# Kernel tuning notes

Hardware: AMD Instinct MI355X
Metric: run time of the kernel (lower is better)

Reference implementation:

```python
import jax, jax.numpy as jnp
import numpy as np

N, E = 20000, 320000
IN_DIM, EDGE_DIM, HID = 64, 16, 64
# (in_c, heads, channels, out_c) per layer; last layer heads=1, concat=False
DIMS = [(64, 4, 64, 256), (256, 4, 64, 256), (256, 1, 64, 64)]


def _ln(x, g, b):
    m = x.mean(-1, keepdims=True)
    v = x.var(-1, keepdims=True)
    return (x - m) / jnp.sqrt(v + 1e-5) * g + b


def _gatv2(x, ei, ea, Wl, bl, Wr, br, We, att, bc, concat):
    # PyG GATv2Conv, eval mode (no dropout), add_self_loops=True, fill_value='mean'
    n = x.shape[0]
    H, C = att.shape
    ar = jnp.arange(n, dtype=ei.dtype)
    src = jnp.concatenate([ei[0], ar])
    dst = jnp.concatenate([ei[1], ar])
    ea_f = jnp.concatenate([ea, jnp.broadcast_to(ea.mean(0), (n, ea.shape[1]))], 0)
    xl = (x @ Wl + bl).reshape(n, H, C)   # source transform
    xr = (x @ Wr + br).reshape(n, H, C)   # target transform
    ee = (ea_f @ We).reshape(-1, H, C)    # edge transform (no bias in PyG)
    e = jax.nn.leaky_relu(xl[src] + xr[dst] + ee, 0.2)       # [E+N, H, C]
    score = jnp.einsum('ehc,hc->eh', e, att)                 # [E+N, H]
    mx = jax.ops.segment_max(score, dst, num_segments=n)
    a = jnp.exp(score - mx[dst])
    a = a / (jax.ops.segment_sum(a, dst, num_segments=n)[dst] + 1e-16)
    out = jax.ops.segment_sum(a[:, :, None] * xl[src], dst, num_segments=n)  # [N,H,C]
    out = out.reshape(n, H * C) if concat else out.mean(1)
    return out + bc


def _forward(x, eis, eas, Wp, bp, gp, bep, layers):
    h = jax.nn.gelu(_ln(x @ Wp + bp, gp, bep), approximate=False)
    for i in range(3):
        Wl, bl, Wr, br, We, att, bc, g, be, Wsk, bsk = layers[i]
        res = h @ Wsk + bsk
        h = _gatv2(h, eis[i], eas[i], Wl, bl, Wr, br, We, att, bc, i < 2)
        h = jax.nn.gelu(_ln(h, g, be), approximate=False) + res
    return h


def setup_inputs() -> dict:
    key = jax.random.key(0)
    ks = iter(jax.random.split(key, 64))
    rn = lambda shape, s=0.05: jax.random.normal(next(ks), shape, jnp.float32) * s
    d = {'x': jax.random.normal(next(ks), (N, IN_DIM), jnp.float32)}
    for i in range(3):
        d['ei%d' % i] = jax.random.randint(next(ks), (2, E), 0, N, jnp.int32)
        d['ea%d' % i] = jax.random.normal(next(ks), (E, EDGE_DIM), jnp.float32)
    d['Wp'] = rn((IN_DIM, HID)); d['bp'] = jnp.zeros(HID)
    d['gp'] = jnp.ones(HID); d['bep'] = jnp.zeros(HID)
    for i, (ic, H, C, oc) in enumerate(DIMS):
        hc = H * C
        d['Wl%d' % i] = rn((ic, hc)); d['bl%d' % i] = jnp.zeros(hc)
        d['Wr%d' % i] = rn((ic, hc)); d['br%d' % i] = jnp.zeros(hc)
        d['We%d' % i] = rn((EDGE_DIM, hc))
        d['att%d' % i] = rn((H, C), 0.1)
        d['bc%d' % i] = jnp.zeros(hc if i < 2 else C)
        d['g%d' % i] = jnp.ones(oc); d['be%d' % i] = jnp.zeros(oc)
        d['Wsk%d' % i] = rn((ic, oc)); d['bsk%d' % i] = jnp.zeros(oc)
    return d


def reference(x, ei0, ea0, ei1, ea1, ei2, ea2, Wp, bp, gp, bep,
              Wl0, bl0, Wr0, br0, We0, att0, bc0, g0, be0, Wsk0, bsk0,
              Wl1, bl1, Wr1, br1, We1, att1, bc1, g1, be1, Wsk1, bsk1,
              Wl2, bl2, Wr2, br2, We2, att2, bc2, g2, be2, Wsk2, bsk2):
    layers = [
        (Wl0, bl0, Wr0, br0, We0, att0, bc0, g0, be0, Wsk0, bsk0),
        (Wl1, bl1, Wr1, br1, We1, att1, bc1, g1, be1, Wsk1, bsk1),
        (Wl2, bl2, Wr2, br2, We2, att2, bc2, g2, be2, Wsk2, bsk2),
    ]
    return _forward(x, (ei0, ei1, ei2), (ea0, ea1, ea2), Wp, bp, gp, bep, layers)
```

## Files before the change

kernel.cpp:

```cpp
#include <hip/hip_runtime.h>
#include <hip/hip_bf16.h>
#include <math.h>

#define NV 20000
#define NE 320000
#define CSR_PAD 16

typedef __attribute__((ext_vector_type(8))) short bf16x8;
typedef __attribute__((ext_vector_type(4))) float f32x4;
typedef __attribute__((ext_vector_type(2))) _Float16 h2;

static __device__ __forceinline__ ushort f2b(float f) {
  __hip_bfloat16 h = __float2bfloat16(f);
  return *reinterpret_cast<ushort*>(&h);
}
static __device__ __forceinline__ float b2f(ushort u) {
  union { ushort s[2]; float f; } c;
  c.s[0] = 0; c.s[1] = u;
  return c.f;
}
static __device__ __forceinline__ ushort f2h(float f) {
  _Float16 h = (_Float16)f;
  return *reinterpret_cast<ushort*>(&h);
}
static __device__ __forceinline__ float blo(unsigned u) { return __uint_as_float(u << 16); }
static __device__ __forceinline__ float bhi(unsigned u) { return __uint_as_float(u & 0xffff0000u); }
static __device__ __forceinline__ h2 u2h2(unsigned u) {
  union { unsigned v; h2 h; } c; c.v = u; return c.h;
}

static __device__ __forceinline__ float wave_sum64(float x) {
  x += __int_as_float(__builtin_amdgcn_update_dpp(0, __float_as_int(x), 0x111, 0xF, 0xF, true));
  x += __int_as_float(__builtin_amdgcn_update_dpp(0, __float_as_int(x), 0x112, 0xF, 0xF, true));
  x += __int_as_float(__builtin_amdgcn_update_dpp(0, __float_as_int(x), 0x114, 0xF, 0xF, true));
  x += __int_as_float(__builtin_amdgcn_update_dpp(0, __float_as_int(x), 0x118, 0xF, 0xF, true));
  x += __int_as_float(__builtin_amdgcn_update_dpp(0, __float_as_int(x), 0x142, 0xA, 0xF, true));
  x += __int_as_float(__builtin_amdgcn_update_dpp(0, __float_as_int(x), 0x143, 0xC, 0xF, true));
  return __int_as_float(__builtin_amdgcn_readlane(__float_as_int(x), 63));
}

static __device__ __forceinline__ float sum16(float x) {
  x += __int_as_float(__builtin_amdgcn_update_dpp(0, __float_as_int(x), 0x121, 0xF, 0xF, true));
  x += __int_as_float(__builtin_amdgcn_update_dpp(0, __float_as_int(x), 0x122, 0xF, 0xF, true));
  x += __int_as_float(__builtin_amdgcn_update_dpp(0, __float_as_int(x), 0x124, 0xF, 0xF, true));
  x += __int_as_float(__builtin_amdgcn_update_dpp(0, __float_as_int(x), 0x128, 0xF, 0xF, true));
  return x;
}

static __device__ __forceinline__ float dot16h_i(const uint4* __restrict__ E,
                                                 const h2* __restrict__ Wch,
                                                 float s) {
#if __has_builtin(__builtin_amdgcn_fdot2)
  const h2* e = (const h2*)E;
#pragma unroll
  for (int j = 0; j < 8; ++j) s = __builtin_amdgcn_fdot2(e[j], Wch[j], s, false);
  return s;
#else
  const unsigned* u = (const unsigned*)E;
#pragma unroll
  for (int j = 0; j < 8; ++j) {
    union { unsigned v; h2 h; } cv; cv.v = u[j];
    s = fmaf((float)cv.h[0], (float)Wch[j][0], s);
    s = fmaf((float)cv.h[1], (float)Wch[j][1], s);
  }
  return s;
#endif
}

struct HArgs {
  const int* ei[3]; int* counts;
  const float* ea[3]; float* easum[3];
};

__global__ __launch_bounds__(256) void hist_kernel(HArgs a) {
  const int t = threadIdx.x, b = (int)blockIdx.x;
  if (b < 3750) {
    int gi = b * 256 + t;
    int l = gi / NE, i = gi - l * NE;
    atomicAdd(&a.counts[(size_t)l * (NV + 1) + a.ei[l][NE + i]], 1);
  } else {
    const int cb = b - 3750;
    const int l = cb >> 8, blk = cb & 255;
    const float4* ea4 = (const float4*)a.ea[l];
    const int cg = t & 3;
    int r = blk * 64 + (t >> 2);
    const int rstride = 256 * 64;
    float4 s = make_float4(0.f, 0.f, 0.f, 0.f);
    for (; r < NE; r += rstride) {
      float4 v = ea4[(size_t)r * 4 + cg];
      s.x += v.x; s.y += v.y; s.z += v.z; s.w += v.w;
    }
    __shared__ float4 red4[256];
    red4[t] = s;
    __syncthreads();
    if (t < 4) {
      float4 tot = make_float4(0.f, 0.f, 0.f, 0.f);
      for (int j = t; j < 256; j += 4) {
        float4 v = red4[j];
        tot.x += v.x; tot.y += v.y; tot.z += v.z; tot.w += v.w;
      }
      atomicAdd(&a.easum[l][t * 4 + 0], tot.x);
      atomicAdd(&a.easum[l][t * 4 + 1], tot.y);
      atomicAdd(&a.easum[l][t * 4 + 2], tot.z);
      atomicAdd(&a.easum[l][t * 4 + 3], tot.w);
    }
  }
}

struct CJob { const float* src; ushort* dst; int K, M; };
struct K2Args {
  const int* counts; int* offs; int* cursor;
  CJob jobs[9];
  unsigned* csr[3]; ushort* eab[3];
  const float *x, *Wp, *bp, *gp, *bep;
  ushort* h0;
  const float* easum;
  const float* We[3];
  unsigned* wchx[3];
  float* esfO[3];
};

__global__ __launch_bounds__(1024) void scan_proj_kernel(K2Args a) {
  const int b = blockIdx.x, t = threadIdx.x;
  if (b < 3) {
    const int* counts = a.counts + b * (NV + 1);
    int* offs = a.offs + b * (NV + 1);
    int* cursor = a.cursor + b * NV;
    __shared__ int ws[16];
    __shared__ int wexcl[17];
    const int lane = t & 63, wid = t >> 6;
    const int base = t * 20;
    int v[20];
    int tot = 0;
#pragma unroll
    for (int j = 0; j < 20; ++j) {
      int i = base + j;
      v[j] = (i < NV) ? counts[i] : 0;
      tot += v[j];
    }
    int x = tot;
#pragma unroll
    for (int o = 1; o < 64; o <<= 1) {
      int yy = __shfl_up(x, o, 64);
      if (lane >= o) x += yy;
    }
    if (lane == 63) ws[wid] = x;
    __syncthreads();
    if (t == 0) {
      int r = 0;
#pragma unroll
      for (int j = 0; j < 16; ++j) { wexcl[j] = r; r += ws[j]; }
      wexcl[16] = r;
    }
    __syncthreads();
    int run = wexcl[wid] + (x - tot);
#pragma unroll
    for (int j = 0; j < 20; ++j) {
      int i = base + j;
      if (i < NV) { offs[i] = run; cursor[i] = run; }
      run += v[j];
    }
    if (t == 0) offs[NV] = wexcl[16];
  } else if (b < 19) {
    if (b == 3 && t < 3 * CSR_PAD) {
      int l = t >> 4, p = t & 15;
      a.csr[l][NE + p] = 0u;
      uint4 z = make_uint4(0, 0, 0, 0);
      *(uint4*)(a.eab[l] + (size_t)(NE + p) * 16) = z;
      *(uint4*)(a.eab[l] + (size_t)(NE + p) * 16 + 8) = z;
    }
#pragma unroll
    for (int j = 0; j < 9; ++j) {
      CJob jb = a.jobs[j];
      const int total = jb.M * jb.K;
      for (int i = (b - 3) * 1024 + t; i < total; i += 16 * 1024) {
        int m = i / jb.K, k = i - m * jb.K;
        jb.dst[i] = f2b(jb.src[(size_t)k * jb.M + m]);
      }
    }
  } else if (b < 19 + NV / 16) {
    const int wid = t >> 6, lane = t & 63;
    const int row = (b - 19) * 16 + wid;
    float xv = a.x[(size_t)row * 64 + lane];
    float acc = a.bp[lane];
#pragma unroll
    for (int k = 0; k < 64; ++k) {
      float v = __shfl(xv, k, 64);
      acc = fmaf(v, a.Wp[k * 64 + lane], acc);
    }
    float s1 = wave_sum64(acc), s2 = wave_sum64(acc * acc);
    float mean = s1 * (1.0f / 64.0f);
    float var  = s2 * (1.0f / 64.0f) - mean * mean;
    float yv = (acc - mean) * rsqrtf(var + 1e-5f) * a.gp[lane] + a.bep[lane];
    float gel = 0.5f * yv * (1.0f + erff(yv * 0.70710678118654752f));
    a.h0[(size_t)row * 64 + lane] = f2b(gel);
  } else {
    for (int i = t; i < 4608; i += 1024) {
      int l, e;
      if (i < 2048)      { l = 0; e = i; }
      else if (i < 4096) { l = 1; e = i - 2048; }
      else               { l = 2; e = i - 4096; }
      const int hcl = (l == 2) ? 64 : 256;
      int k8 = e / hcl, c = e - k8 * hcl;
      const float* We = a.We[l];
      a.wchx[l][e] = (unsigned)f2h(We[(2 * k8) * hcl + c]) |
                     ((unsigned)f2h(We[(2 * k8 + 1) * hcl + c]) << 16);
    }
    for (int i = t; i < 576; i += 1024) {
      int l, c;
      if (i < 256)      { l = 0; c = i; }
      else if (i < 512) { l = 1; c = i - 256; }
      else              { l = 2; c = i - 512; }
      const int hcl = (l == 2) ? 64 : 256;
      const float* We = a.We[l];
      const float* es = a.easum + l * 16;
      float s = 0.f;
#pragma unroll
      for (int k8 = 0; k8 < 8; ++k8) {
        s = fmaf(es[2 * k8], We[(2 * k8) * hcl + c], s);
        s = fmaf(es[2 * k8 + 1], We[(2 * k8 + 1) * hcl + c], s);
      }
      a.esfO[l][c] = s * (1.0f / (float)NE);
    }
  }
}

struct K3Args {
  const ushort *A, *WT;
  const float *b0, *b1, *b2;
  ushort *O0, *O1; float* O2;
  int K, M1, M2, Mtot, NT;
  const int* ei[3]; const float* ea[3];
  int* cursor;
  unsigned* csr[3]; ushort* eab[3]; int HC[3];
};

__global__ __launch_bounds__(256) void mega_kernel(K3Args a) {
  __shared__ ushort As[128][40];
  __shared__ ushort Bs[64][40];
  const int t = threadIdx.x;
  const int b = (int)blockIdx.x;
  if (b < a.NT) {
    const int wave = t >> 6, lane = t & 63;
    const int mcols = a.Mtot >> 6;
    const int col0 = (b % mcols) * 64, row0 = (b / mcols) * 128;
    const int m_ = lane & 15, q = lane >> 4;
    f32x4 acc[2][4];
#pragma unroll
    for (int i = 0; i < 2; ++i)
#pragma unroll
      for (int j = 0; j < 4; ++j) acc[i][j] = (f32x4){0.f, 0.f, 0.f, 0.f};
    const int ar = t >> 1, ac = (t & 1) * 16;
    const int br = t >> 2, bcol = (t & 3) * 8;
    const ushort* Ap = a.A + (size_t)(row0 + ar) * a.K + ac;
    const ushort* Bp = a.WT + (size_t)(col0 + br) * a.K + bcol;
    const bool a_ok = (row0 + ar) < NV;
    for (int k0 = 0; k0 < a.K; k0 += 32) {
      uint4 av0 = make_uint4(0, 0, 0, 0), av1 = make_uint4(0, 0, 0, 0);
      if (a_ok) { av0 = *(const uint4*)(Ap + k0); av1 = *(const uint4*)(Ap + k0 + 8); }
      uint4 bv = *(const uint4*)(Bp + k0);
      *(uint4*)&As[ar][ac] = av0;
      *(uint4*)&As[ar][ac + 8] = av1;
      *(uint4*)&Bs[br][bcol] = bv;
      __syncthreads();
      bf16x8 a0 = *(const bf16x8*)&As[wave * 32 + m_][q * 8];
      bf16x8 a1 = *(const bf16x8*)&As[wave * 32 + 16 + m_][q * 8];
#pragma unroll
      for (int cf = 0; cf < 4; ++cf) {
        bf16x8 bfr = *(const bf16x8*)&Bs[cf * 16 + m_][q * 8];
        acc[0][cf] = __builtin_amdgcn_mfma_f32_16x16x32_bf16(a0, bfr, acc[0][cf], 0, 0, 0);
        acc[1][cf] = __builtin_amdgcn_mfma_f32_16x16x32_bf16(a1, bfr, acc[1][cf], 0, 0, 0);
      }
      __syncthreads();
    }
    const float* bias; int base, mode, Wd;
    if (col0 < a.M1)      { bias = a.b0; base = 0;    mode = 0; Wd = a.M1; }
    else if (col0 < a.M2) { bias = a.b1; base = a.M1; mode = 1; Wd = a.M2 - a.M1; }
    else                  { bias = a.b2; base = a.M2; mode = 2; Wd = a.Mtot - a.M2; }
#pragma unroll
    for (int rf = 0; rf < 2; ++rf) {
#pragma unroll
      for (int cf = 0; cf < 4; ++cf) {
        int col = col0 + cf * 16 + m_ - base;
        float bb = bias[col];
#pragma unroll
        for (int r = 0; r < 4; ++r) {
          int row = row0 + wave * 32 + rf * 16 + q * 4 + r;
          if (row < NV) {
            float v = acc[rf][cf][r] + bb;
            if (mode == 0)      a.O0[(size_t)row * Wd + col] = f2b(v);
            else if (mode == 1) a.O1[(size_t)row * Wd + col] = f2b(v);
            else                a.O2[(size_t)row * Wd + col] = v;
          }
        }
      }
    }
  } else {
    int gi = (b - a.NT) * 256 + t;
    int l = gi / NE, i = gi - l * NE;
    int dst = a.ei[l][NE + i], src = a.ei[l][i];
    int pos = atomicAdd(&a.cursor[(size_t)l * NV + dst], 1);
    a.csr[l][pos] = (unsigned)(src * a.HC[l]);
    const float4* er = (const float4*)(a.ea[l] + (size_t)i * 16);
    float4 q0 = er[0], q1 = er[1], q2 = er[2], q3 = er[3];
    uint4 w0, w1;
    w0.x = (unsigned)f2h(q0.x) | ((unsigned)f2h(q0.y) << 16);
    w0.y = (unsigned)f2h(q0.z) | ((unsigned)f2h(q0.w) << 16);
    w0.z = (unsigned)f2h(q1.x) | ((unsigned)f2h(q1.y) << 16);
    w0.w = (unsigned)f2h(q1.z) | ((unsigned)f2h(q1.w) << 16);
    w1.x = (unsigned)f2h(q2.x) | ((unsigned)f2h(q2.y) << 16);
    w1.y = (unsigned)f2h(q2.z) | ((unsigned)f2h(q2.w) << 16);
    w1.z = (unsigned)f2h(q3.x) | ((unsigned)f2h(q3.y) << 16);
    w1.w = (unsigned)f2h(q3.z) | ((unsigned)f2h(q3.w) << 16);
    *(uint4*)(a.eab[l] + (size_t)pos * 16) = w0;
    *(uint4*)(a.eab[l] + (size_t)pos * 16 + 8) = w1;
  }
}

__global__ __launch_bounds__(256) void gemm_fused(
    const ushort* __restrict__ A, const ushort* __restrict__ WT,
    const float* __restrict__ b0, const float* __restrict__ b1,
    const float* __restrict__ b2,
    ushort* __restrict__ O0, ushort* __restrict__ O1, float* __restrict__ O2,
    int N, int K, int M1, int M2, int Mtot)
{
  __shared__ ushort As[128][40];
  __shared__ ushort Bs[64][40];
  const int t = threadIdx.x, wave = t >> 6, lane = t & 63;
  const int row0 = blockIdx.y * 128, col0 = blockIdx.x * 64;
  const int m_ = lane & 15, q = lane >> 4;
  f32x4 acc[2][4];
#pragma unroll
  for (int i = 0; i < 2; ++i)
#pragma unroll
    for (int j = 0; j < 4; ++j) acc[i][j] = (f32x4){0.f, 0.f, 0.f, 0.f};
  const int ar = t >> 1, ac = (t & 1) * 16;
  const int br = t >> 2, bcol = (t & 3) * 8;
  const ushort* Ap = A + (size_t)(row0 + ar) * K + ac;
  const ushort* Bp = WT + (size_t)(col0 + br) * K + bcol;
  const bool a_ok = (row0 + ar) < N;
  for (int k0 = 0; k0 < K; k0 += 32) {
    uint4 av0 = make_uint4(0, 0, 0, 0), av1 = make_uint4(0, 0, 0, 0);
    if (a_ok) { av0 = *(const uint4*)(Ap + k0); av1 = *(const uint4*)(Ap + k0 + 8); }
    uint4 bv = *(const uint4*)(Bp + k0);
    *(uint4*)&As[ar][ac] = av0;
    *(uint4*)&As[ar][ac + 8] = av1;
    *(uint4*)&Bs[br][bcol] = bv;
    __syncthreads();
    bf16x8 a0 = *(const bf16x8*)&As[wave * 32 + m_][q * 8];
    bf16x8 a1 = *(const bf16x8*)&As[wave * 32 + 16 + m_][q * 8];
#pragma unroll
    for (int cf = 0; cf < 4; ++cf) {
      bf16x8 bfr = *(const bf16x8*)&Bs[cf * 16 + m_][q * 8];
      acc[0][cf] = __builtin_amdgcn_mfma_f32_16x16x32_bf16(a0, bfr, acc[0][cf], 0, 0, 0);
      acc[1][cf] = __builtin_amdgcn_mfma_f32_16x16x32_bf16(a1, bfr, acc[1][cf], 0, 0, 0);
    }
    __syncthreads();
  }
  const float* bias; int base, mode, Wd;
  if (col0 < M1)      { bias = b0; base = 0;  mode = 0; Wd = M1; }
  else if (col0 < M2) { bias = b1; base = M1; mode = 1; Wd = M2 - M1; }
  else                { bias = b2; base = M2; mode = 2; Wd = Mtot - M2; }
#pragma unroll
  for (int rf = 0; rf < 2; ++rf) {
#pragma unroll
    for (int cf = 0; cf < 4; ++cf) {
      int col = col0 + cf * 16 + m_ - base;
      float bb = bias[col];
#pragma unroll
      for (int r = 0; r < 4; ++r) {
        int row = row0 + wave * 32 + rf * 16 + q * 4 + r;
        if (row < N) {
          float v = acc[rf][cf][r] + bb;
          if (mode == 0)      O0[(size_t)row * Wd + col] = f2b(v);
          else if (mode == 1) O1[(size_t)row * Wd + col] = f2b(v);
          else                O2[(size_t)row * Wd + col] = v;
        }
      }
    }
  }
}

__global__ __launch_bounds__(256) void agg4_kernel(
    const ushort* __restrict__ eab, const unsigned* __restrict__ wchx,
    const float* __restrict__ esf,
    const ushort* __restrict__ xl, const ushort* __restrict__ xr,
    const float* __restrict__ att, const float* __restrict__ bc,
    const float* __restrict__ g, const float* __restrict__ be,
    const float* __restrict__ res,
    const int* __restrict__ offs, const unsigned* __restrict__ csr,
    ushort* __restrict__ houtb)
{
  __shared__ float mrg[4][64][5];
  const int t = threadIdx.x, lane = t & 63, wid = t >> 6;
  const int n = blockIdx.x * 2 + (wid >> 1);
  const int par = wid & 1;
  const int cb = 4 * lane;
  const size_t rowb = (size_t)n * 256 + cb;
  const float L2E = 1.4426950408889634f;

  float4 atv = *(const float4*)(att + cb);
  float at[4] = {atv.x * L2E, atv.y * L2E, atv.z * L2E, atv.w * L2E};

  h2 Wch[4][8];
#pragma unroll
  for (int k8 = 0; k8 < 8; ++k8) {
    uint4 wv = *(const uint4*)(wchx + k8 * 256 + cb);
    Wch[0][k8] = u2h2(wv.x); Wch[1][k8] = u2h2(wv.y);
    Wch[2][k8] = u2h2(wv.z); Wch[3][k8] = u2h2(wv.w);
  }
  float4 esfv = *(const float4*)(esf + cb);
  const float* esfp = &esfv.x;

  uint2 qr = *(const uint2*)(xr + rowb);
  float xrv[4] = {blo(qr.x), bhi(qr.x), blo(qr.y), bhi(qr.y)};
  uint2 qn = *(const uint2*)(xl + rowb);
  float xln[4] = {blo(qn.x), bhi(qn.x), blo(qn.y), bhi(qn.y)};

  float acc[4] = {0.f, 0.f, 0.f, 0.f};
  float denom = 0.f;
  if (par == 0) {
    float p = 0.f;
#pragma unroll
    for (int j = 0; j < 4; ++j) {
      float v = xln[j] + xrv[j] + esfp[j];
      v = v > 0.f ? v : 0.2f * v;
      p = fmaf(v, at[j], p);
    }
    float wself = exp2f(sum16(p));
#pragma unroll
    for (int j = 0; j < 4; ++j) acc[j] = wself * xln[j];
    denom = wself;
  }

  const int beg = __builtin_amdgcn_readfirstlane(offs[n]) + par;
  const int end = __builtin_amdgcn_readfirstlane(offs[n + 1]);

  unsigned P[2];
  uint4 EA[2][2];
  uint2 XL[2];
#pragma unroll
  for (int k = 0; k < 2; ++k) {
    P[k] = csr[beg + 2 * k];
    const uint4* ep = (const uint4*)(eab + (size_t)(beg + 2 * k) * 16);
    EA[k][0] = ep[0]; EA[k][1] = ep[1];
  }
#pragma unroll
  for (int k = 0; k < 2; ++k)
    XL[k] = *(const uint2*)(xl + __builtin_amdgcn_readfirstlane(P[k]) + cb);

  for (int idx = beg; idx < end; idx += 4) {
    unsigned Q[2];
    uint4 EB[2][2];
    uint2 XN[2];
#pragma unroll
    for (int k = 0; k < 2; ++k) Q[k] = csr[idx + 4 + 2 * k];
#pragma unroll
    for (int k = 0; k < 2; ++k) {
      const uint4* ep = (const uint4*)(eab + (size_t)(idx + 4 + 2 * k) * 16);
      EB[k][0] = ep[0]; EB[k][1] = ep[1];
    }
#pragma unroll
    for (int k = 0; k < 2; ++k)
      XN[k] = *(const uint2*)(xl + __builtin_amdgcn_readfirstlane(Q[k]) + cb);

#pragma unroll
    for (int k = 0; k < 2; ++k) {
      float xf[4] = {blo(XL[k].x), bhi(XL[k].x), blo(XL[k].y), bhi(XL[k].y)};
      float pp = 0.f;
#pragma unroll
      for (int j = 0; j < 4; ++j) {
        float v = dot16h_i(EA[k], Wch[j], xf[j] + xrv[j]);
        v = v > 0.f ? v : 0.2f * v;
        pp = fmaf(v, at[j], pp);
      }
      float S = sum16(pp);
      float w = (idx + 2 * k < end) ? exp2f(S) : 0.f;
#pragma unroll
      for (int j = 0; j < 4; ++j) acc[j] = fmaf(w, xf[j], acc[j]);
      denom += w;
    }
#pragma unroll
    for (int k = 0; k < 2; ++k) {
      P[k] = Q[k]; EA[k][0] = EB[k][0]; EA[k][1] = EB[k][1]; XL[k] = XN[k];
    }
  }

#pragma unroll
  for (int j = 0; j < 4; ++j) mrg[wid][lane][j] = acc[j];
  mrg[wid][lane][4] = denom;
  __syncthreads();
  const int pw = wid ^ 1;
#pragma unroll
  for (int j = 0; j < 4; ++j) acc[j] += mrg[pw][lane][j];
  denom += mrg[pw][lane][4];
  if (par) return;

  const float inv = 1.0f / (denom + 1e-16f);
  float4 bcv = *(const float4*)(bc + cb);
  float out[4];
  out[0] = acc[0] * inv + bcv.x; out[1] = acc[1] * inv + bcv.y;
  out[2] = acc[2] * inv + bcv.z; out[3] = acc[3] * inv + bcv.w;

  float so1 = out[0] + out[1] + out[2] + out[3];
  float so2 = out[0] * out[0] + out[1] * out[1] + out[2] * out[2] + out[3] * out[3];
  float s1 = wave_sum64(so1), s2 = wave_sum64(so2);
  float mean = s1 * (1.0f / 256.0f);
  float var  = s2 * (1.0f / 256.0f) - mean * mean;
  float rstd = rsqrtf(var + 1e-5f);
  float4 gv = *(const float4*)(g + cb);
  float4 bev = *(const float4*)(be + cb);
  float4 rv = *(const float4*)(res + rowb);
  const float* gp = &gv.x; const float* bep = &bev.x; const float* rp = &rv.x;
  ushort ob[4];
#pragma unroll
  for (int j = 0; j < 4; ++j) {
    float y = (out[j] - mean) * rstd * gp[j] + bep[j];
    float gel = 0.5f * y * (1.0f + erff(y * 0.70710678118654752f));
    ob[j] = f2b(gel + rp[j]);
  }
  uint2 ov;
  ov.x = (unsigned)ob[0] | ((unsigned)ob[1] << 16);
  ov.y = (unsigned)ob[2] | ((unsigned)ob[3] << 16);
  *(uint2*)(houtb + rowb) = ov;
}

__global__ __launch_bounds__(256, 4) void agg1_kernel(
    const ushort* __restrict__ eab, const unsigned* __restrict__ wchx,
    const float* __restrict__ esf,
    const ushort* __restrict__ xl, const ushort* __restrict__ xr,
    const float* __restrict__ att, const float* __restrict__ bc,
    const float* __restrict__ g, const float* __restrict__ be,
    const float* __restrict__ res,
    const int* __restrict__ offs, const unsigned* __restrict__ csr,
    float* __restrict__ houtf)
{
  const int HC = 64;
  __shared__ float mrg[4][64][2];
  const int t = threadIdx.x, lane = t & 63, wid = t >> 6;
  const int n = blockIdx.x * 2 + (wid >> 1);
  const int par = wid & 1;
  const int c = lane;

  const float xr_t = b2f(xr[(size_t)n * HC + c]);
  const float att_t = att[c] * 1.4426950408889634f;
  h2 Wch[8];
#pragma unroll
  for (int k8 = 0; k8 < 8; ++k8) Wch[k8] = u2h2(wchx[k8 * 64 + c]);
  const float eself = esf[c];
  const float xln = b2f(xl[(size_t)n * HC + c]);

  float acc = 0.f, denom = 0.f;
  if (par == 0) {
    float vs = xln + xr_t + eself;
    vs = vs > 0.f ? vs : 0.2f * vs;
    float wself = exp2f(wave_sum64(vs * att_t));
    acc = wself * xln; denom = wself;
  }

  const int beg = __builtin_amdgcn_readfirstlane(offs[n]) + par;
  const int end = __builtin_amdgcn_readfirstlane(offs[n + 1]);

  unsigned P[2];
  uint4 EA[2][2];
  float XL[2];
#pragma unroll
  for (int k = 0; k < 2; ++k) {
    P[k] = csr[beg + 2 * k];
    const uint4* ep = (const uint4*)(eab + (size_t)(beg + 2 * k) * 16);
    EA[k][0] = ep[0]; EA[k][1] = ep[1];
  }
#pragma unroll
  for (int k = 0; k < 2; ++k)
    XL[k] = b2f(xl[__builtin_amdgcn_readfirstlane(P[k]) + c]);

  for (int idx = beg; idx < end; idx += 4) {
    unsigned Q[2];
    uint4 EB[2][2];
    float XLN[2];
#pragma unroll
    for (int k = 0; k < 2; ++k) Q[k] = csr[idx + 4 + 2 * k];
#pragma unroll
    for (int k = 0; k < 2; ++k) {
      const uint4* ep = (const uint4*)(eab + (size_t)(idx + 4 + 2 * k) * 16);
      EB[k][0] = ep[0]; EB[k][1] = ep[1];
    }
#pragma unroll
    for (int k = 0; k < 2; ++k)
      XLN[k] = b2f(xl[__builtin_amdgcn_readfirstlane(Q[k]) + c]);

#pragma unroll
    for (int k = 0; k < 2; ++k) {
      float v = dot16h_i(EA[k], Wch, XL[k] + xr_t);
      v = v > 0.f ? v : 0.2f * v;
      float S = wave_sum64(v * att_t);
      float w = (idx + 2 * k < end) ? exp2f(S) : 0.f;
      acc = fmaf(w, XL[k], acc); denom += w;
    }
#pragma unroll
    for (int k = 0; k < 2; ++k) {
      P[k] = Q[k]; EA[k][0] = EB[k][0]; EA[k][1] = EB[k][1]; XL[k] = XLN[k];
    }
  }

  mrg[wid][lane][0] = acc; mrg[wid][lane][1] = denom;
  __syncthreads();
  acc += mrg[wid ^ 1][lane][0];
  denom += mrg[wid ^ 1][lane][1];
  if (par) return;

  float out = acc / (denom + 1e-16f) + bc[c];
  float s1 = wave_sum64(out), s2 = wave_sum64(out * out);
  float mean = s1 / (float)HC;
  float var  = s2 / (float)HC - mean * mean;
  float y = (out - mean) * rsqrtf(var + 1e-5f) * g[c] + be[c];
  float gel = 0.5f * y * (1.0f + erff(y * 0.70710678118654752f));
  houtf[(size_t)n * HC + c] = gel + res[(size_t)n * HC + c];
}

extern "C" void kernel_launch(void* const* d_in, const int* in_sizes, int n_in,
                              void* d_out, int out_size, void* d_ws, size_t ws_size,
                              hipStream_t stream)
{
  auto in = [&](int i) { return (const float*)d_in[i]; };

  const int ic[3] = {64, 256, 256}, hc[3] = {256, 256, 64}, oc[3] = {256, 256, 64};
  const int CSRN = NE + CSR_PAD;

  char* w = (char*)d_ws;
  size_t off = 0;
  auto alloc = [&](size_t bytes) { void* p = w + off; off = (off + bytes + 511) & ~(size_t)511; return p; };
  ushort* B1   = (ushort*)alloc((size_t)NV * 256 * 2);
  ushort* B2   = (ushort*)alloc((size_t)NV * 256 * 2);
  float*  B3   = (float*)alloc((size_t)NV * 256 * 4);
  ushort* h0bf = (ushort*)alloc((size_t)NV * 64 * 2);
  ushort* h1bf = (ushort*)alloc((size_t)NV * 256 * 2);
  ushort* h2bf = (ushort*)alloc((size_t)NV * 256 * 2);
  ushort* Wcat[3];
  for (int i = 0; i < 3; ++i)
    Wcat[i] = (ushort*)alloc((size_t)(2 * hc[i] + oc[i]) * ic[i] * 2);
  float*    easumA  = (float*)alloc(3 * 64);
  int*      countsA = (int*)alloc((size_t)3 * (NV + 1) * 4);
  int*      offsA   = (int*)alloc((size_t)3 * (NV + 1) * 4);
  int*      cursorA = (int*)alloc((size_t)3 * NV * 4);
  unsigned* csrA    = (unsigned*)alloc((size_t)3 * CSRN * 4);
  ushort*   eabA    = (ushort*)alloc((size_t)3 * CSRN * 16 * 2);
  unsigned* wchxA   = (unsigned*)alloc((size_t)4608 * 4);
  float*    esfA    = (float*)alloc((size_t)576 * 4);

  hipMemsetAsync(easumA, 0, 512 + (size_t)3 * (NV + 1) * 4, stream);

  HArgs ha;
  for (int i = 0; i < 3; ++i) {
    ha.ei[i] = (const int*)d_in[1 + 2 * i];
    ha.ea[i] = in(2 + 2 * i);
    ha.easum[i] = easumA + i * 16;
  }
  ha.counts = countsA;
  hist_kernel<<<3750 + 768, 256, 0, stream>>>(ha);

  K2Args k2;
  k2.counts = countsA; k2.offs = offsA; k2.cursor = cursorA;
  for (int i = 0; i < 3; ++i) {
    k2.jobs[i * 3 + 0] = {in(11 + 11 * i), Wcat[i],                             ic[i], hc[i]};
    k2.jobs[i * 3 + 1] = {in(13 + 11 * i), Wcat[i] + (size_t)hc[i] * ic[i],     ic[i], hc[i]};
    k2.jobs[i * 3 + 2] = {in(20 + 11 * i), Wcat[i] + (size_t)2 * hc[i] * ic[i], ic[i], oc[i]};
    k2.csr[i] = csrA + (size_t)i * CSRN;
    k2.eab[i] = eabA + (size_t)i * CSRN * 16;
    k2.We[i] = in(15 + 11 * i);
  }
  k2.x = in(0); k2.Wp = in(7); k2.bp = in(8); k2.gp = in(9); k2.bep = in(10);
  k2.h0 = h0bf;
  k2.easum = easumA;
  k2.wchx[0] = wchxA; k2.wchx[1] = wchxA + 2048; k2.wchx[2] = wchxA + 4096;
  k2.esfO[0] = esfA; k2.esfO[1] = esfA + 256; k2.esfO[2] = esfA + 512;
  scan_proj_kernel<<<19 + NV / 16 + 1, 1024, 0, stream>>>(k2);

  K3Args ga;
  ga.A = h0bf; ga.WT = Wcat[0];
  ga.b0 = in(12); ga.b1 = in(14); ga.b2 = in(21);
  ga.O0 = B1; ga.O1 = B2; ga.O2 = B3;
  ga.K = 64; ga.M1 = 256; ga.M2 = 512; ga.Mtot = 768;
  ga.NT = (768 / 64) * ((NV + 127) / 128);
  for (int i = 0; i < 3; ++i) {
    ga.ei[i] = (const int*)d_in[1 + 2 * i];
    ga.ea[i] = in(2 + 2 * i);
    ga.csr[i] = csrA + (size_t)i * CSRN;
    ga.eab[i] = eabA + (size_t)i * CSRN * 16;
    ga.HC[i] = hc[i];
  }
  ga.cursor = cursorA;
  mega_kernel<<<ga.NT + 3750, 256, 0, stream>>>(ga);

  agg4_kernel<<<NV / 2, 256, 0, stream>>>(
      eabA + 0, wchxA, esfA, B1, B2, in(16), in(17), in(18), in(19),
      B3, offsA, csrA, h1bf);

  gemm_fused<<<dim3(768 / 64, (NV + 127) / 128), 256, 0, stream>>>(
      h1bf, Wcat[1], in(23), in(25), in(32), B1, B2, B3, NV, 256, 256, 512, 768);

  agg4_kernel<<<NV / 2, 256, 0, stream>>>(
      eabA + (size_t)CSRN * 16, wchxA + 2048, esfA + 256, B1, B2, in(27), in(28),
      in(29), in(30), B3, offsA + (NV + 1), csrA + (size_t)CSRN, h2bf);

  gemm_fused<<<dim3(192 / 64, (NV + 127) / 128), 256, 0, stream>>>(
      h2bf, Wcat[2], in(34), in(36), in(43), B1, B2, B3, NV, 256, 64, 128, 192);

  agg1_kernel<<<NV / 2, 256, 0, stream>>>(
      eabA + (size_t)2 * CSRN * 16, wchxA + 4096, esfA + 512, B1, B2, in(38), in(39),
      in(40), in(41), B3, offsA + 2 * (NV + 1), csrA + (size_t)2 * CSRN,
      (float*)d_out);
}
```

Baseline: 548.0 us.

## Assign one wave per node in aggregation kernels, drop LDS pair merge

The aggregation kernels previously split each destination node's edge list across two waves and merged their partial sums through shared memory with a block barrier. Now a single wave handles all edges of a node, four nodes per block, which removes the LDS merge, the __syncthreads and the idle second wave during the epilogue. The prefetch pipeline is reorganised into a two-stage lookahead on contiguous edges, and agg1 now processes four edges per iteration. Per-wave serial work roughly doubles, so latency hiding depends on the deeper prefetch and on occupancy.

Result: faster. 523.2 us (-4.5%).

```diff
diff --git a/kernel.cpp b/kernel.cpp
--- a/kernel.cpp
+++ b/kernel.cpp
@@ -391,10 +391,8 @@
     const int* __restrict__ offs, const unsigned* __restrict__ csr,
     ushort* __restrict__ houtb)
 {
-  __shared__ float mrg[4][64][5];
-  const int t = threadIdx.x, lane = t & 63, wid = t >> 6;
-  const int n = blockIdx.x * 2 + (wid >> 1);
-  const int par = wid & 1;
+  const int t = threadIdx.x, lane = t & 63, wave = t >> 6;
+  const int n = blockIdx.x * 4 + wave;
   const int cb = 4 * lane;
   const size_t rowb = (size_t)n * 256 + cb;
   const float L2E = 1.4426950408889634f;
@@ -417,52 +415,55 @@
   uint2 qn = *(const uint2*)(xl + rowb);
   float xln[4] = {blo(qn.x), bhi(qn.x), blo(qn.y), bhi(qn.y)};
 
-  float acc[4] = {0.f, 0.f, 0.f, 0.f};
-  float denom = 0.f;
-  if (par == 0) {
-    float p = 0.f;
-#pragma unroll
-    for (int j = 0; j < 4; ++j) {
-      float v = xln[j] + xrv[j] + esfp[j];
-      v = v > 0.f ? v : 0.2f * v;
-      p = fmaf(v, at[j], p);
-    }
-    float wself = exp2f(sum16(p));
-#pragma unroll
-    for (int j = 0; j < 4; ++j) acc[j] = wself * xln[j];
-    denom = wself;
-  }
-
-  const int beg = __builtin_amdgcn_readfirstlane(offs[n]) + par;
+  float p = 0.f;
+#pragma unroll
+  for (int j = 0; j < 4; ++j) {
+    float v = xln[j] + xrv[j] + esfp[j];
+    v = v > 0.f ? v : 0.2f * v;
+    p = fmaf(v, at[j], p);
+  }
+  float wself = exp2f(sum16(p));
+  float acc[4];
+#pragma unroll
+  for (int j = 0; j < 4; ++j) acc[j] = wself * xln[j];
+  float denom = wself;
+
+  const int beg = __builtin_amdgcn_readfirstlane(offs[n]);
   const int end = __builtin_amdgcn_readfirstlane(offs[n + 1]);
 
-  unsigned P[2];
+  unsigned C1[2];
   uint4 EA[2][2];
   uint2 XL[2];
-#pragma unroll
-  for (int k = 0; k < 2; ++k) {
-    P[k] = csr[beg + 2 * k];
-    const uint4* ep = (const uint4*)(eab + (size_t)(beg + 2 * k) * 16);
-    EA[k][0] = ep[0]; EA[k][1] = ep[1];
-  }
-#pragma unroll
-  for (int k = 0; k < 2; ++k)
-    XL[k] = *(const uint2*)(xl + __builtin_amdgcn_readfirstlane(P[k]) + cb);
-
-  for (int idx = beg; idx < end; idx += 4) {
-    unsigned Q[2];
+  {
+    unsigned C0[2];
+#pragma unroll
+    for (int k = 0; k < 2; ++k) C0[k] = csr[beg + k];
+#pragma unroll
+    for (int k = 0; k < 2; ++k) C1[k] = csr[beg + 2 + k];
+#pragma unroll
+    for (int k = 0; k < 2; ++k) {
+      const uint4* ep = (const uint4*)(eab + (size_t)(beg + k) * 16);
+      EA[k][0] = ep[0]; EA[k][1] = ep[1];
+    }
+#pragma unroll
+    for (int k = 0; k < 2; ++k)
+      XL[k] = *(const uint2*)(xl + __builtin_amdgcn_readfirstlane(C0[k]) + cb);
+  }
+
+  for (int idx = beg; idx < end; idx += 2) {
+    unsigned C2[2];
+#pragma unroll
+    for (int k = 0; k < 2; ++k) C2[k] = csr[idx + 4 + k];
     uint4 EB[2][2];
+#pragma unroll
+    for (int k = 0; k < 2; ++k) {
+      const uint4* ep = (const uint4*)(eab + (size_t)(idx + 2 + k) * 16);
+      EB[k][0] = ep[0]; EB[k][1] = ep[1];
+    }
     uint2 XN[2];
 #pragma unroll
-    for (int k = 0; k < 2; ++k) Q[k] = csr[idx + 4 + 2 * k];
-#pragma unroll
-    for (int k = 0; k < 2; ++k) {
-      const uint4* ep = (const uint4*)(eab + (size_t)(idx + 4 + 2 * k) * 16);
-      EB[k][0] = ep[0]; EB[k][1] = ep[1];
-    }
-#pragma unroll
     for (int k = 0; k < 2; ++k)
-      XN[k] = *(const uint2*)(xl + __builtin_amdgcn_readfirstlane(Q[k]) + cb);
+      XN[k] = *(const uint2*)(xl + __builtin_amdgcn_readfirstlane(C1[k]) + cb);
 
 #pragma unroll
     for (int k = 0; k < 2; ++k) {
@@ -475,26 +476,16 @@
         pp = fmaf(v, at[j], pp);
       }
       float S = sum16(pp);
-      float w = (idx + 2 * k < end) ? exp2f(S) : 0.f;
+      float w = (idx + k < end) ? exp2f(S) : 0.f;
 #pragma unroll
       for (int j = 0; j < 4; ++j) acc[j] = fmaf(w, xf[j], acc[j]);
       denom += w;
     }
 #pragma unroll
     for (int k = 0; k < 2; ++k) {
-      P[k] = Q[k]; EA[k][0] = EB[k][0]; EA[k][1] = EB[k][1]; XL[k] = XN[k];
-    }
-  }
-
-#pragma unroll
-  for (int j = 0; j < 4; ++j) mrg[wid][lane][j] = acc[j];
-  mrg[wid][lane][4] = denom;
-  __syncthreads();
-  const int pw = wid ^ 1;
-#pragma unroll
-  for (int j = 0; j < 4; ++j) acc[j] += mrg[pw][lane][j];
-  denom += mrg[pw][lane][4];
-  if (par) return;
+      EA[k][0] = EB[k][0]; EA[k][1] = EB[k][1]; XL[k] = XN[k]; C1[k] = C2[k];
+    }
+  }
 
   const float inv = 1.0f / (denom + 1e-16f);
   float4 bcv = *(const float4*)(bc + cb);
@@ -536,10 +527,8 @@
     float* __restrict__ houtf)
 {
   const int HC = 64;
-  __shared__ float mrg[4][64][2];
-  const int t = threadIdx.x, lane = t & 63, wid = t >> 6;
-  const int n = blockIdx.x * 2 + (wid >> 1);
-  const int par = wid & 1;
+  const int t = threadIdx.x, lane = t & 63, wave = t >> 6;
+  const int n = blockIdx.x * 4 + wave;
   const int c = lane;
 
   const float xr_t = b2f(xr[(size_t)n * HC + c]);
@@ -550,64 +539,63 @@
   const float eself = esf[c];
   const float xln = b2f(xl[(size_t)n * HC + c]);
 
-  float acc = 0.f, denom = 0.f;
-  if (par == 0) {
-    float vs = xln + xr_t + eself;
-    vs = vs > 0.f ? vs : 0.2f * vs;
-    float wself = exp2f(wave_sum64(vs * att_t));
-    acc = wself * xln; denom = wself;
-  }
-
-  const int beg = __builtin_amdgcn_readfirstlane(offs[n]) + par;
+  float vs = xln + xr_t + eself;
+  vs = vs > 0.f ? vs : 0.2f * vs;
+  const float wself = exp2f(wave_sum64(vs * att_t));
+  float acc = wself * xln, denom = wself;
+
+  const int beg = __builtin_amdgcn_readfirstlane(offs[n]);
   const int end = __builtin_amdgcn_readfirstlane(offs[n + 1]);
 
-  unsigned P[2];
-  uint4 EA[2][2];
-  float XL[2];
-#pragma unroll
-  for (int k = 0; k < 2; ++k) {
-    P[k] = csr[beg + 2 * k];
-    const uint4* ep = (const uint4*)(eab + (size_t)(beg + 2 * k) * 16);
-    EA[k][0] = ep[0]; EA[k][1] = ep[1];
-  }
-#pragma unroll
-  for (int k = 0; k < 2; ++k)
-    XL[k] = b2f(xl[__builtin_amdgcn_readfirstlane(P[k]) + c]);
+  unsigned C1[4];
+  uint4 EA[4][2];
+  float XL[4];
+  {
+    unsigned C0[4];
+#pragma unroll
+    for (int k = 0; k < 4; ++k) C0[k] = csr[beg + k];
+#pragma unroll
+    for (int k = 0; k < 4; ++k) C1[k] = csr[beg + 4 + k];
+#pragma unroll
+    for (int k = 0; k < 4; ++k) {
+      const uint4* ep = (const uint4*)(eab + (size_t)(beg + k) * 16);
+      EA[k][0] = ep[0]; EA[k][1] = ep[1];
+    }
+#pragma unroll
+    for (int k = 0; k < 4; ++k)
+      XL[k] = b2f(xl[__builtin_amdgcn_readfirstlane(C0[k]) + c]);
+  }
 
   for (int idx = beg; idx < end; idx += 4) {
-    unsigned Q[2];
-    uint4 EB[2][2];
-    float XLN[2];
-#pragma unroll
-    for (int k = 0; k < 2; ++k) Q[k] = csr[idx + 4 + 2 * k];
-#pragma unroll
-    for (int k = 0; k < 2; ++k) {
-      const uint4* ep = (const uint4*)(eab + (size_t)(idx + 4 + 2 * k) * 16);
+    unsigned C2[4];
+#pragma unroll
+    for (int k = 0; k < 4; ++k) C2[k] = csr[idx + 8 + k];
+    uint4 EB[4][2];
+#pragma unroll
+    for (int k = 0; k < 4; ++k) {
+      const uint4* ep = (const uint4*)(eab + (size_t)(idx + 4 + k) * 16);
       EB[k][0] = ep[0]; EB[k][1] = ep[1];
     }
-#pragma unroll
-    for (int k = 0; k < 2; ++k)
-      XLN[k] = b2f(xl[__builtin_amdgcn_readfirstlane(Q[k]) + c]);
-
-#pragma unroll
-    for (int k = 0; k < 2; ++k) {
+    float XLN[4];
+#pragma unroll
+    for (int k = 0; k < 4; ++k)
+      XLN[k] = b2f(xl[__builtin_amdgcn_readfirstlane(C1[k]) + c]);
+
+    float wv[4];
+#pragma unroll
+    for (int k = 0; k < 4; ++k) {
       float v = dot16h_i(EA[k], Wch, XL[k] + xr_t);
       v = v > 0.f ? v : 0.2f * v;
       float S = wave_sum64(v * att_t);
-      float w = (idx + 2 * k < end) ? exp2f(S) : 0.f;
-      acc = fmaf(w, XL[k], acc); denom += w;
-    }
-#pragma unroll
-    for (int k = 0; k < 2; ++k) {
-      P[k] = Q[k]; EA[k][0] = EB[k][0]; EA[k][1] = EB[k][1]; XL[k] = XLN[k];
-    }
-  }
-
-  mrg[wid][lane][0] = acc; mrg[wid][lane][1] = denom;
-  __syncthreads();
-  acc += mrg[wid ^ 1][lane][0];
-  denom += mrg[wid ^ 1][lane][1];
-  if (par) return;
+      wv[k] = (idx + k < end) ? exp2f(S) : 0.f;
+    }
+#pragma unroll
+    for (int k = 0; k < 4; ++k) { acc = fmaf(wv[k], XL[k], acc); denom += wv[k]; }
+#pragma unroll
+    for (int k = 0; k < 4; ++k) {
+      EA[k][0] = EB[k][0]; EA[k][1] = EB[k][1]; XL[k] = XLN[k]; C1[k] = C2[k];
+    }
+  }
 
   float out = acc / (denom + 1e-16f) + bc[c];
   float s1 = wave_sum64(out), s2 = wave_sum64(out * out);
@@ -692,21 +680,21 @@
   ga.cursor = cursorA;
   mega_kernel<<<ga.NT + 3750, 256, 0, stream>>>(ga);
 
-  agg4_kernel<<<NV / 2, 256, 0, stream>>>(
+  agg4_kernel<<<NV / 4, 256, 0, stream>>>(
       eabA + 0, wchxA, esfA, B1, B2, in(16), in(17), in(18), in(19),
       B3, offsA, csrA, h1bf);
 
   gemm_fused<<<dim3(768 / 64, (NV + 127) / 128), 256, 0, stream>>>(
       h1bf, Wcat[1], in(23), in(25), in(32), B1, B2, B3, NV, 256, 256, 512, 768);
 
-  agg4_kernel<<<NV / 2, 256, 0, stream>>>(
+  agg4_kernel<<<NV / 4, 256, 0, stream>>>(
       eabA + (size_t)CSRN * 16, wchxA + 2048, esfA + 256, B1, B2, in(27), in(28),
       in(29), in(30), B3, offsA + (NV + 1), csrA + (size_t)CSRN, h2bf);
 
   gemm_fused<<<dim3(192 / 64, (NV + 127) / 128), 256, 0, stream>>>(
       h2bf, Wcat[2], in(34), in(36), in(43), B1, B2, B3, NV, 256, 64, 128, 192);
 
-  agg1_kernel<<<NV / 2, 256, 0, stream>>>(
+  agg1_kernel<<<NV / 4, 256, 0, stream>>>(
       eabA + (size_t)2 * CSRN * 16, wchxA + 4096, esfA + 512, B1, B2, in(38), in(39),
       in(40), in(41), B3, offsA + 2 * (NV + 1), csrA + (size_t)2 * CSRN,
       (float*)d_out);
```
